# Performance work log

Measured on AMD Instinct MI355X. Metric: run time of the kernel, lower is better.

The kernel has to match this reference:

```python
import jax, jax.numpy as jnp
import numpy as np

EPS = 1e-5

def _gnn_edge_layer(m, W, b, g, beta, src, dst, n_nodes):
    # DGL send_and_recv(copy_e('m'), sum) : scatter-sum edge feats to dst nodes
    h = jax.ops.segment_sum(m, dst, num_segments=n_nodes)          # [N, d_in]
    # apply_edges: cat(src_h, m) -> Linear -> BatchNorm1d (batch stats) -> relu
    x = jnp.concatenate([h[src], m], axis=1)                        # [E, 2*d_in]
    x = x @ W.T + b                                                 # [E, d_out]
    mu = jnp.mean(x, axis=0)
    var = jnp.var(x, axis=0)                                        # biased, as torch BN training
    x = (x - mu) * jax.lax.rsqrt(var + EPS) * g + beta
    return jax.nn.relu(x), h

def setup_inputs() -> dict:
    key = jax.random.key(0)
    ks = jax.random.split(key, 6)
    E, N = 1_000_000, 100_000
    d0, d1, d2 = 64, 128, 64
    return {
        "m": jax.random.normal(ks[0], (E, d0), jnp.float32),
        "W0": jax.random.normal(ks[1], (d1, 2 * d0), jnp.float32) / np.sqrt(2 * d0),
        "b0": jnp.zeros((d1,), jnp.float32),
        "g0": jnp.ones((d1,), jnp.float32),
        "beta0": jnp.zeros((d1,), jnp.float32),
        "W1": jax.random.normal(ks[2], (d2, 2 * d1), jnp.float32) / np.sqrt(2 * d1),
        "b1": jnp.zeros((d2,), jnp.float32),
        "g1": jnp.ones((d2,), jnp.float32),
        "beta1": jnp.zeros((d2,), jnp.float32),
        "src": jax.random.randint(ks[3], (E,), 0, N, jnp.int32),
        "dst": jax.random.randint(ks[4], (E,), 0, N, jnp.int32),
        "n_nodes": N,
    }

def reference(m, W0, b0, g0, beta0, W1, b1, g1, beta1, src, dst, n_nodes):
    m, h = _gnn_edge_layer(m, W0, b0, g0, beta0, src, dst, n_nodes)
    m, h = _gnn_edge_layer(m, W1, b1, g1, beta1, src, dst, n_nodes)
    # Simple_edge_encoder.forward returns feat_nodes of the last layer
    return h
```

## Files before the change

kernel.cpp:

```cpp
#include <hip/hip_runtime.h>
#include <hip/hip_bf16.h>
#include <stdint.h>


typedef __attribute__((ext_vector_type(8))) short bf16x8;
typedef __attribute__((ext_vector_type(4))) float f32x4;

__device__ inline uint16_t f2bf(float x) {
    uint32_t u = __float_as_uint(x);
    return (uint16_t)((u + 0x7fffu + ((u >> 16) & 1u)) >> 16);
}
__device__ inline float bf2f(uint32_t lo16) { return __uint_as_float(lo16 << 16); }

__global__ __launch_bounds__(256) void k_hist(const int* __restrict__ dst,
                                              int* __restrict__ cnt, int E)
{
    int e = blockIdx.x * 256 + threadIdx.x;
    if (e < E) atomicAdd(&cnt[dst[e]], 1);
}

__global__ __launch_bounds__(256) void k_scanA(const int* __restrict__ cnt,
                                               int* __restrict__ bsum, int N)
{
    int t = threadIdx.x, b = blockIdx.x;
    int i4 = b * 256 + t;
    int4 v = make_int4(0, 0, 0, 0);
    if (i4 < (N >> 2)) v = ((const int4*)cnt)[i4];
    int s = v.x + v.y + v.z + v.w;
    #pragma unroll
    for (int o = 1; o < 64; o <<= 1) s += __shfl_xor(s, o, 64);
    __shared__ int ws[4];
    if ((t & 63) == 0) ws[t >> 6] = s;
    __syncthreads();
    if (t == 0) bsum[b] = ws[0] + ws[1] + ws[2] + ws[3];
}

__global__ __launch_bounds__(128) void k_scanB(int* __restrict__ bsum, int nb)
{
    int t = threadIdx.x;
    int v = (t < nb) ? bsum[t] : 0;
    int lane = t & 63, w = t >> 6;
    int x = v;
    #pragma unroll
    for (int o = 1; o < 64; o <<= 1) {
        int y = __shfl_up(x, o, 64);
        if (lane >= o) x += y;
    }
    __shared__ int wt[2];
    if (lane == 63) wt[w] = x;
    __syncthreads();
    if (w == 1) x += wt[0];
    if (t < nb) bsum[t] = x - v;
}

__global__ __launch_bounds__(256) void k_scanC(const int* __restrict__ cnt,
                                               const int* __restrict__ bsum,
                                               int* __restrict__ off,
                                               int* __restrict__ cur, int N)
{
    int t = threadIdx.x, b = blockIdx.x;
    int i4 = b * 256 + t;
    bool ok = (i4 < (N >> 2));
    int4 v = make_int4(0, 0, 0, 0);
    if (ok) v = ((const int4*)cnt)[i4];
    int s = v.x + v.y + v.z + v.w;
    int lane = t & 63, w = t >> 6;
    int x = s;
    #pragma unroll
    for (int o = 1; o < 64; o <<= 1) {
        int y = __shfl_up(x, o, 64);
        if (lane >= o) x += y;
    }
    __shared__ int wt[4];
    if (lane == 63) wt[w] = x;
    __syncthreads();
    int wbase = 0;
    for (int k = 0; k < w; k++) wbase += wt[k];
    int excl = bsum[b] + wbase + x - s;
    if (ok) {
        int4 o4;
        o4.x = excl; o4.y = excl + v.x; o4.z = o4.y + v.y; o4.w = o4.z + v.z;
        ((int4*)off)[i4] = o4;
        ((int4*)cur)[i4] = o4;
    }
}

__global__ __launch_bounds__(256) void k_perm(const int* __restrict__ dst,
                                              int* __restrict__ cur,
                                              int* __restrict__ perm, int E)
{
    int e = blockIdx.x * 256 + threadIdx.x;
    if (e < E) {
        int pos = atomicAdd(&cur[dst[e]], 1);
        perm[pos] = e;
    }
}

__global__ __launch_bounds__(256) void k1_gather_h1(
    const float* __restrict__ m, const int* __restrict__ perm,
    const int* __restrict__ off, const int* __restrict__ cur,
    ushort* __restrict__ h1bf, int N)
{
    const int lane = threadIdx.x & 63;
    const int n = blockIdx.x * 4 + (threadIdx.x >> 6);
    if (n >= N) return;
    const int s0 = off[n], s1 = cur[n];
    float acc = 0.f;
    for (int i = s0; i < s1; i++) {
        int e = perm[i];
        acc += m[(size_t)e * 64 + lane];
    }
    h1bf[(size_t)n * 64 + lane] = f2bf(acc);
}

template<bool EDGE>
__global__ __launch_bounds__(256) void gemm_mfma(
    const void* __restrict__ Xv,
    const float* __restrict__ W0,
    int wcol,
    const float* __restrict__ bias,
    const float* __restrict__ A,
    const int*   __restrict__ src,
    float* __restrict__ outA,
    ushort* __restrict__ xbf,
    float* __restrict__ gstats,
    int R, int ntiles)
{
    const int t  = threadIdx.x;
    const int l  = t & 63;
    const int lm = l & 15;
    const int q  = l >> 4;
    const int wv = t >> 6;

    bf16x8 bfr[8][2];
    #pragma unroll
    for (int nt = 0; nt < 8; nt++)
        #pragma unroll
        for (int ks = 0; ks < 2; ks++) {
            const float* wp = W0 + (nt * 16 + lm) * 128 + wcol + ks * 32 + q * 8;
            bf16x8 bf;
            #pragma unroll
            for (int j = 0; j < 8; j++) ((ushort*)&bf)[j] = f2bf(wp[j]);
            bfr[nt][ks] = bf;
        }
    float bs[8];
    if (!EDGE) {
        #pragma unroll
        for (int nt = 0; nt < 8; nt++) bs[nt] = bias[nt * 16 + lm];
    }

    __shared__ float sst[256];
    float lsum[8], lsq[8];
    if (EDGE) {
        #pragma unroll
        for (int nt = 0; nt < 8; nt++) { lsum[nt] = 0.f; lsq[nt] = 0.f; }
        sst[t] = 0.f;
        __syncthreads();
    }

    for (int tile = blockIdx.x; tile < ntiles; tile += gridDim.x) {
        const int r0 = tile * 64 + wv * 16;

        bf16x8 af[2];
        if (EDGE) {
            const float* xp = (const float*)Xv + (size_t)(r0 + lm) * 64 + q * 8;
            #pragma unroll
            for (int ks = 0; ks < 2; ks++) {
                float4 w0 = *(const float4*)(xp + ks * 32);
                float4 w1 = *(const float4*)(xp + ks * 32 + 4);
                bf16x8 bf;
                ((ushort*)&bf)[0] = f2bf(w0.x); ((ushort*)&bf)[1] = f2bf(w0.y);
                ((ushort*)&bf)[2] = f2bf(w0.z); ((ushort*)&bf)[3] = f2bf(w0.w);
                ((ushort*)&bf)[4] = f2bf(w1.x); ((ushort*)&bf)[5] = f2bf(w1.y);
                ((ushort*)&bf)[6] = f2bf(w1.z); ((ushort*)&bf)[7] = f2bf(w1.w);
                af[ks] = bf;
            }
        } else {
            const ushort* xp = (const ushort*)Xv + (size_t)(r0 + lm) * 64 + q * 8;
            af[0] = *(const bf16x8*)xp;
            af[1] = *(const bf16x8*)(xp + 32);
        }

        f32x4 acc[8];
        #pragma unroll
        for (int nt = 0; nt < 8; nt++) acc[nt] = (f32x4){0.f, 0.f, 0.f, 0.f};
        #pragma unroll
        for (int ks = 0; ks < 2; ks++)
            #pragma unroll
            for (int nt = 0; nt < 8; nt++)
                acc[nt] = __builtin_amdgcn_mfma_f32_16x16x32_bf16(
                              af[ks], bfr[nt][ks], acc[nt], 0, 0, 0);

        if (!EDGE) {
            #pragma unroll
            for (int r = 0; r < 4; r++) {
                int row = r0 + q * 4 + r;
                if (row < R) {
                    #pragma unroll
                    for (int nt = 0; nt < 8; nt++)
                        outA[(size_t)row * 128 + nt * 16 + lm] = acc[nt][r] + bs[nt];
                }
            }
        } else {
            int4 rA = *(const int4*)(src + r0 + q * 4);
            const int* rAp = &rA.x;
            #pragma unroll
            for (int r = 0; r < 4; r++) {
                int row = r0 + q * 4 + r;
                const float* Ar = A + (size_t)rAp[r] * 128;
                ushort* xo = xbf + (size_t)row * 128 + lm;
                #pragma unroll
                for (int nt = 0; nt < 8; nt++) {
                    float y = acc[nt][r] + Ar[nt * 16 + lm];
                    lsum[nt] += y;
                    lsq[nt]  += y * y;
                    xo[nt * 16] = f2bf(y);
                }
            }
        }
    }

    if (EDGE) {
        #pragma unroll
        for (int nt = 0; nt < 8; nt++) {
            #pragma unroll
            for (int o = 16; o < 64; o <<= 1) {
                lsum[nt] += __shfl_xor(lsum[nt], o, 64);
                lsq[nt]  += __shfl_xor(lsq[nt],  o, 64);
            }
        }
        __syncthreads();
        if (l < 16) {
            #pragma unroll
            for (int nt = 0; nt < 8; nt++) {
                atomicAdd(&sst[nt * 16 + l],       lsum[nt]);
                atomicAdd(&sst[128 + nt * 16 + l], lsq[nt]);
            }
        }
        __syncthreads();
        atomicAdd(&gstats[t], sst[t]);
    }
}

__global__ void k4_finalize(const float* __restrict__ gstats,
                            const float* __restrict__ g0,
                            const float* __restrict__ beta0,
                            float* __restrict__ sc, float Einv)
{
    int j = threadIdx.x;
    float mu  = gstats[j] * Einv;
    float var = gstats[128 + j] * Einv - mu * mu;
    float s   = g0[j] * rsqrtf(var + 1e-5f);
    sc[j]       = s;
    sc[128 + j] = beta0[j] - mu * s;
}

__global__ __launch_bounds__(256) void k5_gather_out(
    const ushort* __restrict__ xbf, const int* __restrict__ perm,
    const int* __restrict__ off, const int* __restrict__ cur,
    const float* __restrict__ sc, float* __restrict__ out, int N)
{
    const int lane = threadIdx.x & 63;
    const int n = blockIdx.x * 4 + (threadIdx.x >> 6);
    if (n >= N) return;
    float2 s = ((const float2*)sc)[lane];
    float2 b = ((const float2*)(sc + 128))[lane];
    const int s0 = off[n], s1 = cur[n];
    float a0 = 0.f, a1 = 0.f;
    for (int i = s0; i < s1; i++) {
        int e = perm[i];
        uint32_t pair = *(const uint32_t*)(xbf + (size_t)e * 128 + 2 * lane);
        a0 += fmaxf(bf2f(pair & 0xffffu) * s.x + b.x, 0.f);
        a1 += fmaxf(bf2f(pair >> 16)     * s.y + b.y, 0.f);
    }
    ((float2*)(out + (size_t)n * 128))[lane] = make_float2(a0, a1);
}

extern "C" void kernel_launch(void* const* d_in, const int* in_sizes, int n_in,
                              void* d_out, int out_size, void* d_ws, size_t ws_size,
                              hipStream_t stream)
{
    const float* m     = (const float*)d_in[0];
    const float* W0    = (const float*)d_in[1];
    const float* b0    = (const float*)d_in[2];
    const float* g0    = (const float*)d_in[3];
    const float* beta0 = (const float*)d_in[4];
    const int*   src   = (const int*)d_in[9];
    const int*   dst   = (const int*)d_in[10];
    float* out = (float*)d_out;

    const int E = in_sizes[0] / 64;
    const int N = out_size / 128;
    const int ntA = (N + 63) / 64;
    const int Npad = ntA * 64;
    const int ntE = E / 64;
    const int nb  = (N + 1023) / 1024;

    auto align = [](size_t x) { return (x + 255) & ~(size_t)255; };
    char* ws = (char*)d_ws;
    size_t o_h1  = 0;
    size_t o_A   = align(o_h1 + (size_t)Npad * 64 * 2);
    size_t o_x   = align(o_A  + (size_t)N * 128 * 4);
    size_t o_gs  = align(o_x  + (size_t)E * 128 * 2);
    size_t o_sc  = align(o_gs + 256 * 4);
    size_t o_cnt = align(o_sc + 256 * 4);
    size_t o_off = align(o_cnt + (size_t)N * 4);
    size_t o_cur = align(o_off + (size_t)N * 4);
    size_t o_pm  = align(o_cur + (size_t)N * 4);
    size_t o_bs  = align(o_pm  + (size_t)E * 4);
    ushort*   h1bf = (ushort*)(ws + o_h1);
    float*    A    = (float*)(ws + o_A);
    ushort*   xbf  = (ushort*)(ws + o_x);
    float*    gs   = (float*)(ws + o_gs);
    float*    sc   = (float*)(ws + o_sc);
    int*      cnt  = (int*)(ws + o_cnt);
    int*      off  = (int*)(ws + o_off);
    int*      cur  = (int*)(ws + o_cur);
    int*      perm = (int*)(ws + o_pm);
    int*      bsum = (int*)(ws + o_bs);

    hipMemsetAsync(cnt, 0, (size_t)N * 4, stream);
    hipMemsetAsync(gs, 0, 256 * 4, stream);

    k_hist<<<(E + 255) / 256, 256, 0, stream>>>(dst, cnt, E);
    k_scanA<<<nb, 256, 0, stream>>>(cnt, bsum, N);
    k_scanB<<<1, 128, 0, stream>>>(bsum, nb);
    k_scanC<<<nb, 256, 0, stream>>>(cnt, bsum, off, cur, N);
    k_perm<<<(E + 255) / 256, 256, 0, stream>>>(dst, cur, perm, E);

    k1_gather_h1<<<(N + 3) / 4, 256, 0, stream>>>(m, perm, off, cur, h1bf, N);

    gemm_mfma<false><<<ntA, 256, 0, stream>>>(h1bf, W0, 0, b0, nullptr, nullptr,
                                              A, nullptr, nullptr, N, ntA);

    gemm_mfma<true><<<2048, 256, 0, stream>>>(m, W0, 64, nullptr, A, src,
                                              nullptr, xbf, gs, E, ntE);

    k4_finalize<<<1, 128, 0, stream>>>(gs, g0, beta0, sc, 1.0f / (float)E);

    k5_gather_out<<<(N + 3) / 4, 256, 0, stream>>>(xbf, perm, off, cur, sc, out, N);
}
```

Measured before the change: 978.0 us.

## Process edges in dst-sorted order so final gather reads contiguous rows

```diff
diff --git a/kernel.cpp b/kernel.cpp
--- a/kernel.cpp
+++ b/kernel.cpp
@@ -99,18 +99,27 @@
 __global__ __launch_bounds__(256) void k1_gather_h1(
     const float* __restrict__ m, const int* __restrict__ perm,
     const int* __restrict__ off, const int* __restrict__ cur,
-    ushort* __restrict__ h1bf, int N)
+    const int* __restrict__ src,
+    ushort* __restrict__ h1bf, int* __restrict__ srcsort, int N)
 {
     const int lane = threadIdx.x & 63;
     const int n = blockIdx.x * 4 + (threadIdx.x >> 6);
     if (n >= N) return;
     const int s0 = off[n], s1 = cur[n];
-    float acc = 0.f;
-    for (int i = s0; i < s1; i++) {
-        int e = perm[i];
-        acc += m[(size_t)e * 64 + lane];
-    }
-    h1bf[(size_t)n * 64 + lane] = f2bf(acc);
+
+    for (int j = s0 + lane; j < s1; j += 64) srcsort[j] = src[perm[j]];
+
+    float a0 = 0.f, a1 = 0.f, a2 = 0.f, a3 = 0.f;
+    int i = s0;
+    for (; i + 4 <= s1; i += 4) {
+        int e0 = perm[i], e1 = perm[i + 1], e2 = perm[i + 2], e3 = perm[i + 3];
+        a0 += m[(size_t)e0 * 64 + lane];
+        a1 += m[(size_t)e1 * 64 + lane];
+        a2 += m[(size_t)e2 * 64 + lane];
+        a3 += m[(size_t)e3 * 64 + lane];
+    }
+    for (; i < s1; i++) a0 += m[(size_t)perm[i] * 64 + lane];
+    h1bf[(size_t)n * 64 + lane] = f2bf((a0 + a1) + (a2 + a3));
 }
 
 template<bool EDGE>
@@ -120,7 +129,8 @@
     int wcol,
     const float* __restrict__ bias,
     const float* __restrict__ A,
-    const int*   __restrict__ src,
+    const int*   __restrict__ srcS,
+    const int*   __restrict__ perm,
     float* __restrict__ outA,
     ushort* __restrict__ xbf,
     float* __restrict__ gstats,
@@ -163,7 +173,8 @@
 
         bf16x8 af[2];
         if (EDGE) {
-            const float* xp = (const float*)Xv + (size_t)(r0 + lm) * 64 + q * 8;
+            const int pr = perm[r0 + lm];
+            const float* xp = (const float*)Xv + (size_t)pr * 64 + q * 8;
             #pragma unroll
             for (int ks = 0; ks < 2; ks++) {
                 float4 w0 = *(const float4*)(xp + ks * 32);
@@ -202,7 +213,7 @@
                 }
             }
         } else {
-            int4 rA = *(const int4*)(src + r0 + q * 4);
+            int4 rA = *(const int4*)(srcS + r0 + q * 4);
             const int* rAp = &rA.x;
             #pragma unroll
             for (int r = 0; r < 4; r++) {
@@ -256,7 +267,7 @@
 }
 
 __global__ __launch_bounds__(256) void k5_gather_out(
-    const ushort* __restrict__ xbf, const int* __restrict__ perm,
+    const ushort* __restrict__ xbf,
     const int* __restrict__ off, const int* __restrict__ cur,
     const float* __restrict__ sc, float* __restrict__ out, int N)
 {
@@ -266,14 +277,30 @@
     float2 s = ((const float2*)sc)[lane];
     float2 b = ((const float2*)(sc + 128))[lane];
     const int s0 = off[n], s1 = cur[n];
-    float a0 = 0.f, a1 = 0.f;
-    for (int i = s0; i < s1; i++) {
-        int e = perm[i];
-        uint32_t pair = *(const uint32_t*)(xbf + (size_t)e * 128 + 2 * lane);
-        a0 += fmaxf(bf2f(pair & 0xffffu) * s.x + b.x, 0.f);
-        a1 += fmaxf(bf2f(pair >> 16)     * s.y + b.y, 0.f);
-    }
-    ((float2*)(out + (size_t)n * 128))[lane] = make_float2(a0, a1);
+    float a0 = 0.f, a1 = 0.f, b0 = 0.f, b1 = 0.f;
+    float c0 = 0.f, c1 = 0.f, d0 = 0.f, d1 = 0.f;
+    int i = s0;
+    for (; i + 4 <= s1; i += 4) {
+        uint32_t p0 = *(const uint32_t*)(xbf + (size_t)i * 128 + 2 * lane);
+        uint32_t p1 = *(const uint32_t*)(xbf + (size_t)(i + 1) * 128 + 2 * lane);
+        uint32_t p2 = *(const uint32_t*)(xbf + (size_t)(i + 2) * 128 + 2 * lane);
+        uint32_t p3 = *(const uint32_t*)(xbf + (size_t)(i + 3) * 128 + 2 * lane);
+        a0 += fmaxf(bf2f(p0 & 0xffffu) * s.x + b.x, 0.f);
+        a1 += fmaxf(bf2f(p0 >> 16)     * s.y + b.y, 0.f);
+        b0 += fmaxf(bf2f(p1 & 0xffffu) * s.x + b.x, 0.f);
+        b1 += fmaxf(bf2f(p1 >> 16)     * s.y + b.y, 0.f);
+        c0 += fmaxf(bf2f(p2 & 0xffffu) * s.x + b.x, 0.f);
+        c1 += fmaxf(bf2f(p2 >> 16)     * s.y + b.y, 0.f);
+        d0 += fmaxf(bf2f(p3 & 0xffffu) * s.x + b.x, 0.f);
+        d1 += fmaxf(bf2f(p3 >> 16)     * s.y + b.y, 0.f);
+    }
+    for (; i < s1; i++) {
+        uint32_t p = *(const uint32_t*)(xbf + (size_t)i * 128 + 2 * lane);
+        a0 += fmaxf(bf2f(p & 0xffffu) * s.x + b.x, 0.f);
+        a1 += fmaxf(bf2f(p >> 16)     * s.y + b.y, 0.f);
+    }
+    ((float2*)(out + (size_t)n * 128))[lane] =
+        make_float2((a0 + b0) + (c0 + d0), (a1 + b1) + (c1 + d1));
 }
 
 extern "C" void kernel_launch(void* const* d_in, const int* in_sizes, int n_in,
@@ -308,6 +335,7 @@
     size_t o_cur = align(o_off + (size_t)N * 4);
     size_t o_pm  = align(o_cur + (size_t)N * 4);
     size_t o_bs  = align(o_pm  + (size_t)E * 4);
+    size_t o_ss  = align(o_bs  + 1024 * 4);
     ushort*   h1bf = (ushort*)(ws + o_h1);
     float*    A    = (float*)(ws + o_A);
     ushort*   xbf  = (ushort*)(ws + o_x);
@@ -318,6 +346,7 @@
     int*      cur  = (int*)(ws + o_cur);
     int*      perm = (int*)(ws + o_pm);
     int*      bsum = (int*)(ws + o_bs);
+    int*      srcs = (int*)(ws + o_ss);
 
     hipMemsetAsync(cnt, 0, (size_t)N * 4, stream);
     hipMemsetAsync(gs, 0, 256 * 4, stream);
@@ -328,15 +357,16 @@
     k_scanC<<<nb, 256, 0, stream>>>(cnt, bsum, off, cur, N);
     k_perm<<<(E + 255) / 256, 256, 0, stream>>>(dst, cur, perm, E);
 
-    k1_gather_h1<<<(N + 3) / 4, 256, 0, stream>>>(m, perm, off, cur, h1bf, N);
+    k1_gather_h1<<<(N + 3) / 4, 256, 0, stream>>>(m, perm, off, cur, src,
+                                                  h1bf, srcs, N);
 
     gemm_mfma<false><<<ntA, 256, 0, stream>>>(h1bf, W0, 0, b0, nullptr, nullptr,
-                                              A, nullptr, nullptr, N, ntA);
-
-    gemm_mfma<true><<<2048, 256, 0, stream>>>(m, W0, 64, nullptr, A, src,
+                                              nullptr, A, nullptr, nullptr, N, ntA);
+
+    gemm_mfma<true><<<2048, 256, 0, stream>>>(m, W0, 64, nullptr, A, srcs, perm,
                                               nullptr, xbf, gs, E, ntE);
 
     k4_finalize<<<1, 128, 0, stream>>>(gs, g0, beta0, sc, 1.0f / (float)E);
 
-    k5_gather_out<<<(N + 3) / 4, 256, 0, stream>>>(xbf, perm, off, cur, sc, out, N);
-}
+    k5_gather_out<<<(N + 3) / 4, 256, 0, stream>>>(xbf, off, cur, sc, out, N);
+}
```

New measurement: 824.1 us. 1.19x faster.
